# Kernel tuning notes

Hardware: AMD Instinct MI355X
Metric: run time of the kernel (lower is better)

The kernel has to match this reference:

```python
import jax, jax.numpy as jnp
import numpy as np

B, C, H, W = 8, 64, 64, 64


def _conv1x1(x, Wm, b):
    # 1x1 conv == per-pixel channel matmul: (O,C) x (B,C,H,W) -> (B,O,H,W)
    return jnp.einsum('oc,bchw->bohw', Wm, x) + b[:, None, None]


def setup_inputs() -> dict:
    key = jax.random.key(0)
    ks = jax.random.split(key, 9)
    s = 1.0 / np.sqrt(C)  # torch Conv2d default init scale
    return {
        'x': jax.random.normal(ks[0], (B, C, H, W), dtype=jnp.float32),
        'Wq': jax.random.normal(ks[1], (C, C), dtype=jnp.float32) * s,
        'bq': jax.random.normal(ks[2], (C,), dtype=jnp.float32) * s,
        'Wk': jax.random.normal(ks[3], (C, C), dtype=jnp.float32) * s,
        'bk': jax.random.normal(ks[4], (C,), dtype=jnp.float32) * s,
        'Wv': jax.random.normal(ks[5], (C, C), dtype=jnp.float32) * s,
        'bv': jax.random.normal(ks[6], (C,), dtype=jnp.float32) * s,
        'Wo': jax.random.normal(ks[7], (C, C), dtype=jnp.float32) * s,
        'bo': jax.random.normal(ks[8], (C,), dtype=jnp.float32) * s,
    }


def reference(x, Wq, bq, Wk, bk, Wv, bv, Wo, bo):
    b_, c_, h_, w_ = x.shape
    n = h_ * w_
    q = _conv1x1(x, Wq, bq).reshape(b_, c_, n)  # (B,C,N)
    k = _conv1x1(x, Wk, bk).reshape(b_, c_, n)
    v = _conv1x1(x, Wv, bv).reshape(b_, c_, n)
    # scores = q^T k  (no 1/sqrt(d) scaling, per original)
    scores = jnp.einsum('bci,bcj->bij', q, k)          # (B,N,N)
    attn = jax.nn.softmax(scores, axis=-1)
    # res = bmm(v, attn): res[b,c,i] = sum_j v[b,c,j] * attn[b,j,i] (swapped order)
    res = jnp.einsum('bcj,bji->bci', v, attn).reshape(b_, c_, h_, w_)
    return _conv1x1(res, Wo, bo) + res
```

## Files before the change

### kernel.cpp

```cpp
#include <hip/hip_runtime.h>
#include <stdint.h>

#define NPIX 4096
#define LOG2E 1.44269504088896340736f

typedef __bf16 bf16x8 __attribute__((ext_vector_type(8)));
typedef float  f32x4  __attribute__((ext_vector_type(4)));
typedef unsigned long long ull;

union FragU {
  bf16x8 f;
  uint4  u;
  ull    q[2];
  unsigned short s[8];
};

static __device__ __forceinline__ unsigned short f2bf(float x) {
  unsigned int u = __float_as_uint(x);
  u += 0x7FFFu + ((u >> 16) & 1u);
  return (unsigned short)(u >> 16);
}
static __device__ __forceinline__ float bf2f(unsigned short s) {
  return __uint_as_float(((unsigned int)s) << 16);
}
static __device__ __forceinline__ unsigned int pack2(unsigned short a, unsigned short b) {
  return (unsigned int)a | ((unsigned int)b << 16);
}
static __device__ __forceinline__ float e2(float x) { return __builtin_amdgcn_exp2f(x); }

static __device__ __forceinline__ bf16x8 load_frag(const unsigned short* base, int byteOff) {
  const char* p = reinterpret_cast<const char*>(base) + byteOff;
  uint2 a = *reinterpret_cast<const uint2*>(p);
  uint2 b = *reinterpret_cast<const uint2*>(p + 32);
  FragU fu;
  fu.u = make_uint4(a.x, a.y, b.x, b.y);
  return fu.f;
}

static __device__ __forceinline__ int pib(int row, int beta) {
  return ((beta + 2 * (row & 7)) & 15) ^ ((row >> 3) & 1);
}

static __device__ __forceinline__ bf16x8 lds_frag(const char* base, int row, int cb) {
  const int rb = row << 7;
  ull a = *reinterpret_cast<const ull*>(base + rb + (pib(row, cb >> 3) << 3));
  ull b = *reinterpret_cast<const ull*>(base + rb + (pib(row, (cb + 32) >> 3) << 3));
  FragU fu;
  fu.q[0] = a; fu.q[1] = b;
  return fu.f;
}

static __device__ __forceinline__ void stage_write(char* dst, int t, uint4 r0, uint4 r1) {
  const int o0 = t * 16, o1 = 4096 + t * 16;
  const int w0 = o0 >> 7, w1 = o1 >> 7;
  const int e0 = ((((o0 & 127) >> 3) + 2 * (w0 & 7)) & 15);
  const int e1 = ((((o1 & 127) >> 3) + 2 * (w1 & 7)) & 15);
  const uint4 a0 = ((w0 >> 3) & 1) ? make_uint4(r0.z, r0.w, r0.x, r0.y) : r0;
  const uint4 a1 = ((w1 >> 3) & 1) ? make_uint4(r1.z, r1.w, r1.x, r1.y) : r1;
  *reinterpret_cast<uint4*>(dst + (w0 << 7) + (e0 << 3)) = a0;
  *reinterpret_cast<uint4*>(dst + (w1 << 7) + (e1 << 3)) = a1;
}

__global__ __launch_bounds__(256) void qkv_proj(
    const float* __restrict__ x,
    const float* __restrict__ Wq, const float* __restrict__ bq,
    const float* __restrict__ Wk, const float* __restrict__ bk,
    const float* __restrict__ Wv, const float* __restrict__ bv,
    unsigned short* __restrict__ qT, unsigned short* __restrict__ kT,
    unsigned short* __restrict__ vC)
{
  const int t  = threadIdx.x;
  const int b  = blockIdx.y;
  const int n  = blockIdx.x * 256 + t;
  const int o0 = blockIdx.z * 16;

  float xv[64];
  #pragma unroll
  for (int c = 0; c < 64; ++c) xv[c] = x[((size_t)b * 64 + c) * NPIX + n];

  const float* Wp[3] = {Wq, Wk, Wv};
  const float* Bp[3] = {bq, bk, bv};

  #pragma unroll
  for (int p = 0; p < 3; ++p) {
    const float* W  = Wp[p];
    const float* Bv = Bp[p];
    unsigned short outv[16];
    #pragma unroll
    for (int oo = 0; oo < 16; ++oo) {
      float acc = Bv[o0 + oo];
      #pragma unroll
      for (int c = 0; c < 64; ++c) acc += W[(o0 + oo) * 64 + c] * xv[c];
      if (p == 0) acc *= LOG2E;
      outv[oo] = f2bf(acc);
    }
    if (p < 2) {
      unsigned short* dst = (p == 0 ? qT : kT) + ((size_t)b * NPIX + n) * 64 + o0;
      uint4 w0 = make_uint4(pack2(outv[0], outv[1]),  pack2(outv[2], outv[3]),
                            pack2(outv[4], outv[5]),  pack2(outv[6], outv[7]));
      uint4 w1 = make_uint4(pack2(outv[8], outv[9]),  pack2(outv[10], outv[11]),
                            pack2(outv[12], outv[13]), pack2(outv[14], outv[15]));
      *reinterpret_cast<uint4*>(dst)     = w0;
      *reinterpret_cast<uint4*>(dst + 8) = w1;
    } else {
      #pragma unroll
      for (int oo = 0; oo < 16; ++oo)
        vC[((size_t)b * 64 + o0 + oo) * NPIX + n] = outv[oo];
    }
  }
}

__global__ __launch_bounds__(256, 2) void attn_rowsum(
    const unsigned short* __restrict__ qT, const unsigned short* __restrict__ kT,
    float* __restrict__ Zpart, int ntiles)
{
  __shared__ __align__(16) char sK[2 * 8192];

  const int t    = threadIdx.x;
  const int b    = blockIdx.y;
  const int part = blockIdx.z;
  const int lane = t & 63;
  const int wv   = t >> 6;
  const int j0   = blockIdx.x * 256 + wv * 64;
  const int lr   = lane & 15;
  const int lg   = lane >> 4;

  bf16x8 aq0[4], aq1[4];
  #pragma unroll
  for (int f = 0; f < 4; ++f) {
    const unsigned short* qrow = qT + ((size_t)b * NPIX + j0 + f * 16 + lr) * 64;
    aq0[f] = load_frag(qrow, lg * 8);
    aq1[f] = load_frag(qrow, 64 + lg * 8);
  }

  const char* kbase = reinterpret_cast<const char*>(kT) + (size_t)b * NPIX * 128
                      + (size_t)part * ntiles * 8192;

  float zacc[4][4];
  #pragma unroll
  for (int f = 0; f < 4; ++f)
    #pragma unroll
    for (int r = 0; r < 4; ++r) zacc[f][r] = 0.f;

  uint4 r0 = *reinterpret_cast<const uint4*>(kbase + t * 16);
  uint4 r1 = *reinterpret_cast<const uint4*>(kbase + 4096 + t * 16);

  for (int tile = 0; tile < ntiles; ++tile) {
    char* buf = sK + (tile & 1) * 8192;
    stage_write(buf, t, r0, r1);
    __syncthreads();
    if (tile + 1 < ntiles) {
      const char* src = kbase + (size_t)(tile + 1) * 8192;
      r0 = *reinterpret_cast<const uint4*>(src + t * 16);
      r1 = *reinterpret_cast<const uint4*>(src + 4096 + t * 16);
    }
    bf16x8 kf0[4], kf1[4];
    #pragma unroll
    for (int s = 0; s < 4; ++s) {
      kf0[s] = lds_frag(buf, s * 16 + lr, lg * 8);
      kf1[s] = lds_frag(buf, s * 16 + lr, 64 + lg * 8);
    }
    #pragma unroll
    for (int f = 0; f < 4; ++f) {
      #pragma unroll
      for (int s = 0; s < 4; ++s) {
        f32x4 S = {0.f, 0.f, 0.f, 0.f};
        S = __builtin_amdgcn_mfma_f32_16x16x32_bf16(aq0[f], kf0[s], S, 0, 0, 0);
        S = __builtin_amdgcn_mfma_f32_16x16x32_bf16(aq1[f], kf1[s], S, 0, 0, 0);
        zacc[f][0] += e2(S[0]);
        zacc[f][1] += e2(S[1]);
        zacc[f][2] += e2(S[2]);
        zacc[f][3] += e2(S[3]);
      }
    }
    __syncthreads();
  }

  #pragma unroll
  for (int f = 0; f < 4; ++f) {
    #pragma unroll
    for (int m = 8; m >= 1; m >>= 1) {
      #pragma unroll
      for (int r = 0; r < 4; ++r) zacc[f][r] += __shfl_xor(zacc[f][r], m, 64);
    }
  }
  if (lr == 0) {
    float* dst = Zpart + ((size_t)part * 8 + b) * NPIX + j0 + lg * 4;
    #pragma unroll
    for (int f = 0; f < 4; ++f) {
      #pragma unroll
      for (int r = 0; r < 4; ++r) dst[f * 16 + r] = zacc[f][r];
    }
  }
}

__global__ __launch_bounds__(256) void vscale(
    unsigned short* __restrict__ vC, const float* __restrict__ Zpart, int nparts)
{
  const int idx = blockIdx.x * 256 + threadIdx.x;
  const int jc  = idx & 511;
  const int b   = idx >> 15;
  unsigned short* p = vC + (size_t)idx * 8;
  const float* zb = Zpart + (size_t)b * NPIX + jc * 8;
  float z[8];
  #pragma unroll
  for (int e = 0; e < 8; ++e) z[e] = 0.f;
  for (int pp = 0; pp < nparts; ++pp) {
    const float* zp = zb + (size_t)pp * 8 * NPIX;
    #pragma unroll
    for (int e = 0; e < 8; ++e) z[e] += zp[e];
  }
  FragU v;
  v.q[0] = reinterpret_cast<const ull*>(p)[0];
  v.q[1] = reinterpret_cast<const ull*>(p)[1];
  #pragma unroll
  for (int e = 0; e < 8; ++e) v.s[e] = f2bf(bf2f(v.s[e]) * (1.0f / z[e]));
  reinterpret_cast<ull*>(p)[0] = v.q[0];
  reinterpret_cast<ull*>(p)[1] = v.q[1];
}

__global__ __launch_bounds__(256, 2) void attn_pv(
    const unsigned short* __restrict__ qT, const unsigned short* __restrict__ kT,
    const unsigned short* __restrict__ vC, unsigned short* __restrict__ resP,
    int ntiles)
{
  __shared__ __align__(16) char sQ[2 * 8192];
  __shared__ __align__(16) char sV[2 * 8192];

  const int t    = threadIdx.x;
  const int b    = blockIdx.y;
  const int part = blockIdx.z;
  const int lane = t & 63;
  const int wv   = t >> 6;
  const int i0   = blockIdx.x * 256 + wv * 64;
  const int lr   = lane & 15;
  const int lg   = lane >> 4;
  const int jstart = part * ntiles * 64;

  bf16x8 kf0[4], kf1[4];
  #pragma unroll
  for (int s = 0; s < 4; ++s) {
    const unsigned short* krow = kT + ((size_t)b * NPIX + i0 + s * 16 + lr) * 64;
    kf0[s] = load_frag(krow, lg * 8);
    kf1[s] = load_frag(krow, 64 + lg * 8);
  }

  const char* qbase = reinterpret_cast<const char*>(qT) + ((size_t)b * NPIX + jstart) * 128;
  const char* vbase = reinterpret_cast<const char*>(vC) + (size_t)b * 64 * 8192
                      + (size_t)jstart * 2;

  const int vo0_row = (t * 16) >> 7,        vo0_col = (t * 16) & 127;
  const int vo1_row = (4096 + t * 16) >> 7, vo1_col = (4096 + t * 16) & 127;

  f32x4 acc[4][4];
  #pragma unroll
  for (int m = 0; m < 4; ++m)
    #pragma unroll
    for (int s = 0; s < 4; ++s) acc[m][s] = (f32x4){0.f, 0.f, 0.f, 0.f};

  uint4 q0 = *reinterpret_cast<const uint4*>(qbase + t * 16);
  uint4 q1 = *reinterpret_cast<const uint4*>(qbase + 4096 + t * 16);
  uint4 v0 = *reinterpret_cast<const uint4*>(vbase + (size_t)vo0_row * 8192 + vo0_col);
  uint4 v1 = *reinterpret_cast<const uint4*>(vbase + (size_t)vo1_row * 8192 + vo1_col);

  for (int tile = 0; tile < ntiles; ++tile) {
    char* Qt = sQ + (tile & 1) * 8192;
    char* Vt = sV + (tile & 1) * 8192;
    stage_write(Qt, t, q0, q1);
    stage_write(Vt, t, v0, v1);
    __syncthreads();
    if (tile + 1 < ntiles) {
      const char* qsrc = qbase + (size_t)(tile + 1) * 8192;
      q0 = *reinterpret_cast<const uint4*>(qsrc + t * 16);
      q1 = *reinterpret_cast<const uint4*>(qsrc + 4096 + t * 16);
      const int jb = (tile + 1) * 128;
      v0 = *reinterpret_cast<const uint4*>(vbase + (size_t)vo0_row * 8192 + jb + vo0_col);
      v1 = *reinterpret_cast<const uint4*>(vbase + (size_t)vo1_row * 8192 + jb + vo1_col);
    }

    bf16x8 qf0[4], qf1[4], vf0[4], vf1[4];
    #pragma unroll
    for (int f = 0; f < 4; ++f) {
      qf0[f] = lds_frag(Qt, f * 16 + lr, lg * 8);
      qf1[f] = lds_frag(Qt, f * 16 + lr, 64 + lg * 8);
    }
    #pragma unroll
    for (int m = 0; m < 4; ++m) {
      vf0[m] = lds_frag(Vt, m * 16 + lr, lg * 8);
      vf1[m] = lds_frag(Vt, m * 16 + lr, 64 + lg * 8);
    }

    #pragma unroll
    for (int s = 0; s < 4; ++s) {
      f32x4 sj[4];
      #pragma unroll
      for (int f = 0; f < 4; ++f) {
        sj[f] = (f32x4){0.f, 0.f, 0.f, 0.f};
        sj[f] = __builtin_amdgcn_mfma_f32_16x16x32_bf16(qf0[f], kf0[s], sj[f], 0, 0, 0);
        sj[f] = __builtin_amdgcn_mfma_f32_16x16x32_bf16(qf1[f], kf1[s], sj[f], 0, 0, 0);
      }
      FragU pe0, pe1;
      #pragma unroll
      for (int r = 0; r < 4; ++r) {
        pe0.f[r]     = (__bf16)e2(sj[0][r]);
        pe0.f[4 + r] = (__bf16)e2(sj[1][r]);
        pe1.f[r]     = (__bf16)e2(sj[2][r]);
        pe1.f[4 + r] = (__bf16)e2(sj[3][r]);
      }
      #pragma unroll
      for (int m = 0; m < 4; ++m) {
        acc[m][s] = __builtin_amdgcn_mfma_f32_16x16x32_bf16(vf0[m], pe0.f, acc[m][s], 0, 0, 0);
        acc[m][s] = __builtin_amdgcn_mfma_f32_16x16x32_bf16(vf1[m], pe1.f, acc[m][s], 0, 0, 0);
      }
    }
    __syncthreads();
  }

  unsigned short* rbase = resP + ((size_t)part * 8 + b) * 64 * NPIX;
  #pragma unroll
  for (int m = 0; m < 4; ++m) {
    #pragma unroll
    for (int s = 0; s < 4; ++s) {
      #pragma unroll
      for (int r = 0; r < 4; ++r) {
        rbase[(size_t)(m * 16 + lg * 4 + r) * NPIX + i0 + s * 16 + lr] = f2bf(acc[m][s][r]);
      }
    }
  }
}

__global__ __launch_bounds__(256) void resred(
    const unsigned short* __restrict__ resP, float* __restrict__ res, int nparts)
{
  const size_t idx = (size_t)blockIdx.x * 256 + threadIdx.x;
  const uint4* src = reinterpret_cast<const uint4*>(resP) + idx;
  float a[8];
  #pragma unroll
  for (int e = 0; e < 8; ++e) a[e] = 0.f;
  for (int p = 0; p < nparts; ++p) {
    FragU u;
    u.u = src[(size_t)p * 262144];
    #pragma unroll
    for (int e = 0; e < 8; ++e) a[e] += bf2f(u.s[e]);
  }
  float4 o0 = make_float4(a[0], a[1], a[2], a[3]);
  float4 o1 = make_float4(a[4], a[5], a[6], a[7]);
  reinterpret_cast<float4*>(res)[idx * 2]     = o0;
  reinterpret_cast<float4*>(res)[idx * 2 + 1] = o1;
}

__global__ __launch_bounds__(256) void out_proj(
    const float* __restrict__ res, const float* __restrict__ Wo,
    const float* __restrict__ bo, float* __restrict__ out)
{
  const int t  = threadIdx.x;
  const int b  = blockIdx.y;
  const int n  = blockIdx.x * 256 + t;
  const int o0 = blockIdx.z * 16;

  float rv[64];
  #pragma unroll
  for (int c = 0; c < 64; ++c) rv[c] = res[((size_t)b * 64 + c) * NPIX + n];

  #pragma unroll
  for (int oo = 0; oo < 16; ++oo) {
    float acc = bo[o0 + oo];
    #pragma unroll
    for (int c = 0; c < 64; ++c) acc += Wo[(o0 + oo) * 64 + c] * rv[c];
    acc += res[((size_t)b * 64 + o0 + oo) * NPIX + n];
    out[((size_t)b * 64 + o0 + oo) * NPIX + n] = acc;
  }
}

extern "C" void kernel_launch(void* const* d_in, const int* in_sizes, int n_in,
                              void* d_out, int out_size, void* d_ws, size_t ws_size,
                              hipStream_t stream) {
  const float* x  = (const float*)d_in[0];
  const float* Wq = (const float*)d_in[1];
  const float* bq = (const float*)d_in[2];
  const float* Wk = (const float*)d_in[3];
  const float* bk = (const float*)d_in[4];
  const float* Wv = (const float*)d_in[5];
  const float* bv = (const float*)d_in[6];
  const float* Wo = (const float*)d_in[7];
  const float* bo = (const float*)d_in[8];
  float* out = (float*)d_out;

  char* ws = (char*)d_ws;
  unsigned short* qT   = (unsigned short*)(ws);
  unsigned short* kT   = (unsigned short*)(ws + ((size_t)4 << 20));
  float* res           = (float*)(ws);
  unsigned short* vC   = (unsigned short*)(ws + ((size_t)8 << 20));
  float* Zpart         = (float*)(ws + ((size_t)12 << 20));
  unsigned short* resP = (unsigned short*)(ws + ((size_t)13 << 20));

  int nparts;
  const size_t MB = (size_t)1 << 20;
  if      (ws_size >= 13 * MB + 8 * 4 * MB) nparts = 8;
  else if (ws_size >= 13 * MB + 4 * 4 * MB) nparts = 4;
  else if (ws_size >= 13 * MB + 2 * 4 * MB) nparts = 2;
  else                                      nparts = 1;
  const int ntiles = 64 / nparts;

  qkv_proj<<<dim3(16, 8, 4), 256, 0, stream>>>(x, Wq, bq, Wk, bk, Wv, bv, qT, kT, vC);
  attn_rowsum<<<dim3(16, 8, nparts), 256, 0, stream>>>(qT, kT, Zpart, ntiles);
  vscale<<<dim3(1024), 256, 0, stream>>>(vC, Zpart, nparts);
  attn_pv<<<dim3(16, 8, nparts), 256, 0, stream>>>(qT, kT, vC, resP, ntiles);
  resred<<<dim3(1024), 256, 0, stream>>>(resP, res, nparts);
  out_proj<<<dim3(16, 8, 4), 256, 0, stream>>>(res, Wo, bo, out);
}
```

Before: 213.9 us.

## Drop second barrier per tile and fold softmax normalization into P

Both attention loops now write the next K/Q/V tile into the alternate LDS buffer after compute, which removes the trailing __syncthreads per tile and keeps a two-deep register prefetch. The vscale pass that rescaled V in bf16 is replaced by a small zred kernel that stores reciprocal row sums. attn_pv then multiplies each exponentiated score by that reciprocal before the bf16 conversion. This trades one bandwidth-bound V rewrite for extra multiplies and float4 loads in the inner loop, and it changes rounding slightly.

```diff
diff --git a/kernel.cpp b/kernel.cpp
--- a/kernel.cpp
+++ b/kernel.cpp
@@ -144,16 +144,15 @@
 
   uint4 r0 = *reinterpret_cast<const uint4*>(kbase + t * 16);
   uint4 r1 = *reinterpret_cast<const uint4*>(kbase + 4096 + t * 16);
+  stage_write(sK, t, r0, r1);
+  if (ntiles > 1) {
+    r0 = *reinterpret_cast<const uint4*>(kbase + 8192 + t * 16);
+    r1 = *reinterpret_cast<const uint4*>(kbase + 8192 + 4096 + t * 16);
+  }
 
   for (int tile = 0; tile < ntiles; ++tile) {
-    char* buf = sK + (tile & 1) * 8192;
-    stage_write(buf, t, r0, r1);
     __syncthreads();
-    if (tile + 1 < ntiles) {
-      const char* src = kbase + (size_t)(tile + 1) * 8192;
-      r0 = *reinterpret_cast<const uint4*>(src + t * 16);
-      r1 = *reinterpret_cast<const uint4*>(src + 4096 + t * 16);
-    }
+    const char* buf = sK + (tile & 1) * 8192;
     bf16x8 kf0[4], kf1[4];
     #pragma unroll
     for (int s = 0; s < 4; ++s) {
@@ -173,7 +172,14 @@
         zacc[f][3] += e2(S[3]);
       }
     }
-    __syncthreads();
+    if (tile + 1 < ntiles) {
+      stage_write(sK + ((tile + 1) & 1) * 8192, t, r0, r1);
+      if (tile + 2 < ntiles) {
+        const char* src = kbase + (size_t)(tile + 2) * 8192;
+        r0 = *reinterpret_cast<const uint4*>(src + t * 16);
+        r1 = *reinterpret_cast<const uint4*>(src + 4096 + t * 16);
+      }
+    }
   }
 
   #pragma unroll
@@ -194,35 +200,19 @@
   }
 }
 
-__global__ __launch_bounds__(256) void vscale(
-    unsigned short* __restrict__ vC, const float* __restrict__ Zpart, int nparts)
+__global__ __launch_bounds__(256) void zred(
+    float* __restrict__ Zpart, int nparts)
 {
   const int idx = blockIdx.x * 256 + threadIdx.x;
-  const int jc  = idx & 511;
-  const int b   = idx >> 15;
-  unsigned short* p = vC + (size_t)idx * 8;
-  const float* zb = Zpart + (size_t)b * NPIX + jc * 8;
-  float z[8];
-  #pragma unroll
-  for (int e = 0; e < 8; ++e) z[e] = 0.f;
-  for (int pp = 0; pp < nparts; ++pp) {
-    const float* zp = zb + (size_t)pp * 8 * NPIX;
-    #pragma unroll
-    for (int e = 0; e < 8; ++e) z[e] += zp[e];
-  }
-  FragU v;
-  v.q[0] = reinterpret_cast<const ull*>(p)[0];
-  v.q[1] = reinterpret_cast<const ull*>(p)[1];
-  #pragma unroll
-  for (int e = 0; e < 8; ++e) v.s[e] = f2bf(bf2f(v.s[e]) * (1.0f / z[e]));
-  reinterpret_cast<ull*>(p)[0] = v.q[0];
-  reinterpret_cast<ull*>(p)[1] = v.q[1];
+  float z = 0.f;
+  for (int p = 0; p < nparts; ++p) z += Zpart[(size_t)p * 8 * NPIX + idx];
+  Zpart[idx] = 1.0f / z;
 }
 
 __global__ __launch_bounds__(256, 2) void attn_pv(
     const unsigned short* __restrict__ qT, const unsigned short* __restrict__ kT,
-    const unsigned short* __restrict__ vC, unsigned short* __restrict__ resP,
-    int ntiles)
+    const unsigned short* __restrict__ vC, const float* __restrict__ rcpZ,
+    unsigned short* __restrict__ resP, int ntiles)
 {
   __shared__ __align__(16) char sQ[2 * 8192];
   __shared__ __align__(16) char sV[2 * 8192];
@@ -248,6 +238,7 @@
   const char* qbase = reinterpret_cast<const char*>(qT) + ((size_t)b * NPIX + jstart) * 128;
   const char* vbase = reinterpret_cast<const char*>(vC) + (size_t)b * 64 * 8192
                       + (size_t)jstart * 2;
+  const float* rzbase = rcpZ + (size_t)b * NPIX + jstart + lg * 4;
 
   const int vo0_row = (t * 16) >> 7,        vo0_col = (t * 16) & 127;
   const int vo1_row = (4096 + t * 16) >> 7, vo1_col = (4096 + t * 16) & 127;
@@ -262,21 +253,25 @@
   uint4 q1 = *reinterpret_cast<const uint4*>(qbase + 4096 + t * 16);
   uint4 v0 = *reinterpret_cast<const uint4*>(vbase + (size_t)vo0_row * 8192 + vo0_col);
   uint4 v1 = *reinterpret_cast<const uint4*>(vbase + (size_t)vo1_row * 8192 + vo1_col);
+  stage_write(sQ, t, q0, q1);
+  stage_write(sV, t, v0, v1);
+  if (ntiles > 1) {
+    q0 = *reinterpret_cast<const uint4*>(qbase + 8192 + t * 16);
+    q1 = *reinterpret_cast<const uint4*>(qbase + 8192 + 4096 + t * 16);
+    v0 = *reinterpret_cast<const uint4*>(vbase + (size_t)vo0_row * 8192 + 128 + vo0_col);
+    v1 = *reinterpret_cast<const uint4*>(vbase + (size_t)vo1_row * 8192 + 128 + vo1_col);
+  }
 
   for (int tile = 0; tile < ntiles; ++tile) {
-    char* Qt = sQ + (tile & 1) * 8192;
-    char* Vt = sV + (tile & 1) * 8192;
-    stage_write(Qt, t, q0, q1);
-    stage_write(Vt, t, v0, v1);
     __syncthreads();
-    if (tile + 1 < ntiles) {
-      const char* qsrc = qbase + (size_t)(tile + 1) * 8192;
-      q0 = *reinterpret_cast<const uint4*>(qsrc + t * 16);
-      q1 = *reinterpret_cast<const uint4*>(qsrc + 4096 + t * 16);
-      const int jb = (tile + 1) * 128;
-      v0 = *reinterpret_cast<const uint4*>(vbase + (size_t)vo0_row * 8192 + jb + vo0_col);
-      v1 = *reinterpret_cast<const uint4*>(vbase + (size_t)vo1_row * 8192 + jb + vo1_col);
-    }
+    const char* Qt = sQ + (tile & 1) * 8192;
+    const char* Vt = sV + (tile & 1) * 8192;
+
+    const float* rzt = rzbase + tile * 64;
+    float4 rz0 = *reinterpret_cast<const float4*>(rzt);
+    float4 rz1 = *reinterpret_cast<const float4*>(rzt + 16);
+    float4 rz2 = *reinterpret_cast<const float4*>(rzt + 32);
+    float4 rz3 = *reinterpret_cast<const float4*>(rzt + 48);
 
     bf16x8 qf0[4], qf1[4], vf0[4], vf1[4];
     #pragma unroll
@@ -302,10 +297,10 @@
       FragU pe0, pe1;
       #pragma unroll
       for (int r = 0; r < 4; ++r) {
-        pe0.f[r]     = (__bf16)e2(sj[0][r]);
-        pe0.f[4 + r] = (__bf16)e2(sj[1][r]);
-        pe1.f[r]     = (__bf16)e2(sj[2][r]);
-        pe1.f[4 + r] = (__bf16)e2(sj[3][r]);
+        pe0.f[r]     = (__bf16)(e2(sj[0][r]) * (&rz0.x)[r]);
+        pe0.f[4 + r] = (__bf16)(e2(sj[1][r]) * (&rz1.x)[r]);
+        pe1.f[r]     = (__bf16)(e2(sj[2][r]) * (&rz2.x)[r]);
+        pe1.f[4 + r] = (__bf16)(e2(sj[3][r]) * (&rz3.x)[r]);
       }
       #pragma unroll
       for (int m = 0; m < 4; ++m) {
@@ -313,7 +308,19 @@
         acc[m][s] = __builtin_amdgcn_mfma_f32_16x16x32_bf16(vf1[m], pe1.f, acc[m][s], 0, 0, 0);
       }
     }
-    __syncthreads();
+
+    if (tile + 1 < ntiles) {
+      stage_write(sQ + ((tile + 1) & 1) * 8192, t, q0, q1);
+      stage_write(sV + ((tile + 1) & 1) * 8192, t, v0, v1);
+      if (tile + 2 < ntiles) {
+        const char* qsrc = qbase + (size_t)(tile + 2) * 8192;
+        q0 = *reinterpret_cast<const uint4*>(qsrc + t * 16);
+        q1 = *reinterpret_cast<const uint4*>(qsrc + 4096 + t * 16);
+        const int jb = (tile + 2) * 128;
+        v0 = *reinterpret_cast<const uint4*>(vbase + (size_t)vo0_row * 8192 + jb + vo0_col);
+        v1 = *reinterpret_cast<const uint4*>(vbase + (size_t)vo1_row * 8192 + jb + vo1_col);
+      }
+    }
   }
 
   unsigned short* rbase = resP + ((size_t)part * 8 + b) * 64 * NPIX;
@@ -404,8 +411,8 @@
 
   qkv_proj<<<dim3(16, 8, 4), 256, 0, stream>>>(x, Wq, bq, Wk, bk, Wv, bv, qT, kT, vC);
   attn_rowsum<<<dim3(16, 8, nparts), 256, 0, stream>>>(qT, kT, Zpart, ntiles);
-  vscale<<<dim3(1024), 256, 0, stream>>>(vC, Zpart, nparts);
-  attn_pv<<<dim3(16, 8, nparts), 256, 0, stream>>>(qT, kT, vC, resP, ntiles);
+  zred<<<dim3(128), 256, 0, stream>>>(Zpart, nparts);
+  attn_pv<<<dim3(16, 8, nparts), 256, 0, stream>>>(qT, kT, vC, Zpart , resP, ntiles);
   resred<<<dim3(1024), 256, 0, stream>>>(resP, res, nparts);
   out_proj<<<dim3(16, 8, 4), 256, 0, stream>>>(res, Wo, bo, out);
 }
```

Result: slower. 224.1 us (+4.8%).
